# Performance work log

Hardware: AMD Instinct MI355X
Metric: run time of the kernel (lower is better)

The kernel has to match this reference:

```python
import jax, jax.numpy as jnp
import numpy as np

EPS = 1e-6
H = 64
SIGMA = 0.02


def setup_inputs() -> dict:
    key = jax.random.key(0)
    x = jax.random.normal(key, (8, 3, 65536), dtype=jnp.float32)
    return {"x": x}


def reference(x):
    # x: (B, 3, N) in roughly [-1, 1]; map to [0, 1]
    x = jnp.clip(x / 2.0 + 0.5, 0.0, 1.0)
    I = jnp.transpose(x, (0, 2, 1))  # (B, N, 3)
    # intensity scale I_y (intensity_scale=True)
    Iy = jnp.sqrt(jnp.sum(I * I, axis=-1, keepdims=True) + EPS)  # (B, N, 1)
    lin = jnp.linspace(-3.0, 3.0, H, dtype=I.dtype)  # (h,)
    logI = jnp.log(I + EPS)  # (B, N, 3)
    # log-chromaticity coordinates
    Iu = logI - logI[..., jnp.array([1, 0, 0])]  # (B, N, 3)
    Iv = logI - logI[..., jnp.array([2, 2, 1])]  # (B, N, 3)
    # inverse-quadratic kernel over bins: (B, N, 3, h)
    du = jnp.abs(Iu[..., None] - lin)
    dv = jnp.abs(Iv[..., None] - lin)
    ku = 1.0 / (1.0 + jnp.square(du) / (SIGMA ** 2))
    kv = 1.0 / (1.0 + jnp.square(dv) / (SIGMA ** 2))
    wu = Iy[..., None] * ku  # (B, N, 3, h)
    # reduce over pixels via batched outer product -> (B, 3, h, h)
    hists = jnp.einsum('bnch,bncg->bchg', wu, kv)
    return hists / (jnp.sum(hists, axis=(1, 2, 3), keepdims=True) + EPS)
```

## Files before the change

### kernel.cpp

```cpp
#include <hip/hip_runtime.h>
#include <hip/hip_bf16.h>


typedef __bf16 bf16x8 __attribute__((ext_vector_type(8)));
typedef float  f32x4  __attribute__((ext_vector_type(4)));

constexpr int   HBINS = 64;
constexpr float EPSF  = 1e-6f;
constexpr int   BATCH = 8;
constexpr int   NPIX  = 65536;
constexpr int   NBC   = 24;
constexpr int   CHUNKS = 32;
constexpr int   PPC   = NPIX / CHUNKS;
constexpr int   ROUNDS = PPC / 256;
constexpr float BINSTEP  = 300.0f / 63.0f;
constexpr float LOGSCALE = 34.6573590279973f;

__global__ __launch_bounds__(256, 3) void hist_kernel(const float* __restrict__ x,
                                                      float* __restrict__ ws) {
    const int bc   = blockIdx.y;
    const int b    = bc / 3;
    const int c    = bc - b * 3;
    const int t    = threadIdx.x;
    const int lane = t & 63;
    const int w    = t >> 6;
    const int kgrp = lane >> 4;
    const int l16  = lane & 15;

    __shared__ float cu_s[2][256];
    __shared__ float cv_s[2][256];
    __shared__ float iy_s[2][256];
    __shared__ float lhist[HBINS * HBINS];

    for (int i = t; i < HBINS * HBINS; i += 256) lhist[i] = 0.0f;

    f32x4 acc[4][4];
#pragma unroll
    for (int m = 0; m < 4; ++m)
#pragma unroll
        for (int n = 0; n < 4; ++n) acc[m][n] = (f32x4){0.f, 0.f, 0.f, 0.f};

    const float* xr = x + ((size_t)b * 3 + 0) * NPIX;
    const float* xg = x + ((size_t)b * 3 + 1) * NPIX;
    const float* xb = x + ((size_t)b * 3 + 2) * NPIX;
    const int pix0 = blockIdx.x * PPC;

    auto produce = [&](float r, float g, float bl, float& cu, float& cv, float& iy) {
        r  = fminf(fmaxf(fmaf(r,  0.5f, 0.5f), 0.0f), 1.0f);
        g  = fminf(fmaxf(fmaf(g,  0.5f, 0.5f), 0.0f), 1.0f);
        bl = fminf(fmaxf(fmaf(bl, 0.5f, 0.5f), 0.0f), 1.0f);
        const float l2r = __log2f(r  + EPSF);
        const float l2g = __log2f(g  + EPSF);
        const float l2b = __log2f(bl + EPSF);
        float lc, lu, lv;
        if (c == 0)      { lc = l2r; lu = l2g; lv = l2b; }
        else if (c == 1) { lc = l2g; lu = l2r; lv = l2b; }
        else             { lc = l2b; lu = l2r; lv = l2g; }
        cu = (lc - lu) * LOGSCALE;
        cv = (lc - lv) * LOGSCALE;
        iy = __builtin_amdgcn_sqrtf(fmaf(r, r, fmaf(g, g, fmaf(bl, bl, EPSF))));
    };

    {
        float cu, cv, iy;
        produce(xr[pix0 + t], xg[pix0 + t], xb[pix0 + t], cu, cv, iy);
        cu_s[0][t] = cu; cv_s[0][t] = cv; iy_s[0][t] = iy;
    }
    __syncthreads();

    for (int rnd = 0; rnd < ROUNDS; ++rnd) {
        const int cur = rnd & 1;
        const int nxt = cur ^ 1;
        const bool have_next = (rnd + 1 < ROUNDS);

        float rn = 0.f, gn = 0.f, bn = 0.f;
        if (have_next) {
            const int p = pix0 + (rnd + 1) * 256 + t;
            rn = xr[p]; gn = xg[p]; bn = xb[p];
        }

#pragma unroll
        for (int ks = 0; ks < 2; ++ks) {
            const int k0 = w * 64 + ks * 32 + kgrp * 8;
            float cu8[8], cv8[8], iy8[8];
            *(float4*)&cu8[0] = *(const float4*)&cu_s[cur][k0];
            *(float4*)&cu8[4] = *(const float4*)&cu_s[cur][k0 + 4];
            *(float4*)&cv8[0] = *(const float4*)&cv_s[cur][k0];
            *(float4*)&cv8[4] = *(const float4*)&cv_s[cur][k0 + 4];
            *(float4*)&iy8[0] = *(const float4*)&iy_s[cur][k0];
            *(float4*)&iy8[4] = *(const float4*)&iy_s[cur][k0 + 4];

            bf16x8 bfr[4];
#pragma unroll
            for (int n = 0; n < 4; ++n) {
                const float ling = (float)(n * 16 + l16) * BINSTEP - 150.0f;
#pragma unroll
                for (int j = 0; j < 8; ++j) {
                    const float d = cv8[j] - ling;
                    bfr[n][j] = (__bf16)__builtin_amdgcn_rcpf(fmaf(d, d, 1.0f));
                }
            }
#pragma unroll
            for (int m = 0; m < 4; ++m) {
                const float linh = (float)(m * 16 + l16) * BINSTEP - 150.0f;
                bf16x8 af;
#pragma unroll
                for (int j = 0; j < 8; ++j) {
                    const float d = cu8[j] - linh;
                    af[j] = (__bf16)(iy8[j] * __builtin_amdgcn_rcpf(fmaf(d, d, 1.0f)));
                }
#pragma unroll
                for (int n = 0; n < 4; ++n)
                    acc[m][n] = __builtin_amdgcn_mfma_f32_16x16x32_bf16(af, bfr[n], acc[m][n], 0, 0, 0);
            }
        }

        if (have_next) {
            float cu, cv, iy;
            produce(rn, gn, bn, cu, cv, iy);
            cu_s[nxt][t] = cu; cv_s[nxt][t] = cv; iy_s[nxt][t] = iy;
        }
        __syncthreads();
    }

    const int crow = kgrp * 4;
#pragma unroll
    for (int m = 0; m < 4; ++m)
#pragma unroll
        for (int n = 0; n < 4; ++n)
#pragma unroll
            for (int ri = 0; ri < 4; ++ri)
                atomicAdd(&lhist[(m * 16 + crow + ri) * HBINS + n * 16 + l16], acc[m][n][ri]);
    __syncthreads();

    float* gh = ws + (size_t)bc * HBINS * HBINS;
    for (int i = t; i < HBINS * HBINS; i += 256) atomicAdd(&gh[i], lhist[i]);
}

__global__ __launch_bounds__(256) void norm_kernel(const float* __restrict__ ws,
                                                   float* __restrict__ out) {
    const int b = blockIdx.x;
    const float* h = ws  + (size_t)b * 3 * HBINS * HBINS;
    float*       o = out + (size_t)b * 3 * HBINS * HBINS;
    const int t = threadIdx.x;
    const int n = 3 * HBINS * HBINS;

    float s = 0.0f;
    for (int i = t; i < n; i += 256) s += h[i];
#pragma unroll
    for (int off = 32; off > 0; off >>= 1) s += __shfl_down(s, off, 64);

    __shared__ float partial[4];
    if ((t & 63) == 0) partial[t >> 6] = s;
    __syncthreads();
    const float total = partial[0] + partial[1] + partial[2] + partial[3];
    const float inv = 1.0f / (total + EPSF);

    for (int i = t; i < n; i += 256) o[i] = h[i] * inv;
}

extern "C" void kernel_launch(void* const* d_in, const int* in_sizes, int n_in,
                              void* d_out, int out_size, void* d_ws, size_t ws_size,
                              hipStream_t stream) {
    const float* x   = (const float*)d_in[0];
    float*       out = (float*)d_out;
    float*       ws  = (float*)d_ws;

    hipMemsetAsync(ws, 0, (size_t)NBC * HBINS * HBINS * sizeof(float), stream);

    dim3 grid(CHUNKS, NBC);
    hist_kernel<<<grid, 256, 0, stream>>>(x, ws);
    norm_kernel<<<BATCH, 256, 0, stream>>>(ws, out);
}
```

Baseline: 169.7 us.

## Write per-block private histograms instead of global atomics, reduce in norm kernel

Each hist block now stores its 64x64 partial histogram to its own workspace slot with plain vectorized stores, which also removes the memset, when the workspace is large enough. Otherwise atomics are spread over 8 copies per (batch, channel) to cut contention. The norm kernel then sums the copies while normalizing. This removes global atomic contention but makes the norm kernel, which runs only 8 blocks, read 32x more data (about 12.6MB).

```diff
diff --git a/kernel.cpp b/kernel.cpp
--- a/kernel.cpp
+++ b/kernel.cpp
@@ -6,10 +6,12 @@
 typedef float  f32x4  __attribute__((ext_vector_type(4)));
 
 constexpr int   HBINS = 64;
+constexpr int   HB2   = HBINS * HBINS;
 constexpr float EPSF  = 1e-6f;
 constexpr int   BATCH = 8;
 constexpr int   NPIX  = 65536;
 constexpr int   NBC   = 24;
+constexpr int   NCOPY = 8;
 constexpr int   CHUNKS = 32;
 constexpr int   PPC   = NPIX / CHUNKS;
 constexpr int   ROUNDS = PPC / 256;
@@ -17,7 +19,8 @@
 constexpr float LOGSCALE = 34.6573590279973f;
 
 __global__ __launch_bounds__(256, 3) void hist_kernel(const float* __restrict__ x,
-                                                      float* __restrict__ ws) {
+                                                      float* __restrict__ ws,
+                                                      int priv) {
     const int bc   = blockIdx.y;
     const int b    = bc / 3;
     const int c    = bc - b * 3;
@@ -30,9 +33,9 @@
     __shared__ float cu_s[2][256];
     __shared__ float cv_s[2][256];
     __shared__ float iy_s[2][256];
-    __shared__ float lhist[HBINS * HBINS];
+    __shared__ float lhist[HB2];
 
-    for (int i = t; i < HBINS * HBINS; i += 256) lhist[i] = 0.0f;
+    for (int i = t; i < HB2; i += 256) lhist[i] = 0.0f;
 
     f32x4 acc[4][4];
 #pragma unroll
@@ -133,20 +136,27 @@
                 atomicAdd(&lhist[(m * 16 + crow + ri) * HBINS + n * 16 + l16], acc[m][n][ri]);
     __syncthreads();
 
-    float* gh = ws + (size_t)bc * HBINS * HBINS;
-    for (int i = t; i < HBINS * HBINS; i += 256) atomicAdd(&gh[i], lhist[i]);
+    if (priv) {
+        float* gh = ws + ((size_t)bc * CHUNKS + blockIdx.x) * HB2;
+        for (int i = t * 4; i < HB2; i += 1024)
+            *(float4*)&gh[i] = *(const float4*)&lhist[i];
+    } else {
+        float* gh = ws + ((size_t)bc * NCOPY + (blockIdx.x & (NCOPY - 1))) * HB2;
+        for (int i = t; i < HB2; i += 256) atomicAdd(&gh[i], lhist[i]);
+    }
 }
 
 __global__ __launch_bounds__(256) void norm_kernel(const float* __restrict__ ws,
-                                                   float* __restrict__ out) {
+                                                   float* __restrict__ out,
+                                                   int ncopy) {
     const int b = blockIdx.x;
-    const float* h = ws  + (size_t)b * 3 * HBINS * HBINS;
-    float*       o = out + (size_t)b * 3 * HBINS * HBINS;
+    const float* h = ws  + (size_t)b * 3 * ncopy * HB2;
+    float*       o = out + (size_t)b * 3 * HB2;
     const int t = threadIdx.x;
-    const int n = 3 * HBINS * HBINS;
+    const int n = 3 * HB2;
 
     float s = 0.0f;
-    for (int i = t; i < n; i += 256) s += h[i];
+    for (int i = t; i < 3 * ncopy * HB2; i += 256) s += h[i];
 #pragma unroll
     for (int off = 32; off > 0; off >>= 1) s += __shfl_down(s, off, 64);
 
@@ -156,7 +166,14 @@
     const float total = partial[0] + partial[1] + partial[2] + partial[3];
     const float inv = 1.0f / (total + EPSF);
 
-    for (int i = t; i < n; i += 256) o[i] = h[i] * inv;
+    for (int i = t; i < n; i += 256) {
+        const int c  = i >> 12;
+        const int hg = i & 4095;
+        float v = 0.0f;
+        for (int k = 0; k < ncopy; ++k)
+            v += h[((size_t)c * ncopy + k) * HB2 + hg];
+        o[i] = v * inv;
+    }
 }
 
 extern "C" void kernel_launch(void* const* d_in, const int* in_sizes, int n_in,
@@ -166,9 +183,14 @@
     float*       out = (float*)d_out;
     float*       ws  = (float*)d_ws;
 
-    hipMemsetAsync(ws, 0, (size_t)NBC * HBINS * HBINS * sizeof(float), stream);
+    const size_t priv_bytes = (size_t)NBC * CHUNKS * HB2 * sizeof(float);
+    const bool   priv       = ws_size >= priv_bytes;
+
+    if (!priv) {
+        hipMemsetAsync(ws, 0, (size_t)NBC * NCOPY * HB2 * sizeof(float), stream);
+    }
 
     dim3 grid(CHUNKS, NBC);
-    hist_kernel<<<grid, 256, 0, stream>>>(x, ws);
-    norm_kernel<<<BATCH, 256, 0, stream>>>(ws, out);
+    hist_kernel<<<grid, 256, 0, stream>>>(x, ws, priv ? 1 : 0);
+    norm_kernel<<<BATCH, 256, 0, stream>>>(ws, out, priv ? CHUNKS : NCOPY);
 }
```

After: 663.3 us. 3.91x slower.

## Spread global histogram atomics over replicated copies and parallelize normalization

Applied to the files above, without the earlier changes.

The hist kernel now writes its per-block histogram into one of eight replicated copies per (batch, channel), so fewer blocks contend on the same global addresses. A new reduce kernel, spread over 96 blocks, sums the copies, writes the raw histogram to the output and atomically accumulates per-batch totals. A separate scale kernel then normalizes with float4 accesses. This replaces the single 8-block norm kernel, but it adds a launch, a larger memset and extra workspace traffic.

```diff
diff --git a/kernel.cpp b/kernel.cpp
--- a/kernel.cpp
+++ b/kernel.cpp
@@ -6,13 +6,16 @@
 typedef float  f32x4  __attribute__((ext_vector_type(4)));
 
 constexpr int   HBINS = 64;
+constexpr int   HB2   = HBINS * HBINS;
 constexpr float EPSF  = 1e-6f;
 constexpr int   BATCH = 8;
 constexpr int   NPIX  = 65536;
 constexpr int   NBC   = 24;
+constexpr int   NCOPY = 8;
 constexpr int   CHUNKS = 32;
 constexpr int   PPC   = NPIX / CHUNKS;
 constexpr int   ROUNDS = PPC / 256;
+constexpr int   SEGS  = 4;
 constexpr float BINSTEP  = 300.0f / 63.0f;
 constexpr float LOGSCALE = 34.6573590279973f;
 
@@ -30,9 +33,9 @@
     __shared__ float cu_s[2][256];
     __shared__ float cv_s[2][256];
     __shared__ float iy_s[2][256];
-    __shared__ float lhist[HBINS * HBINS];
-
-    for (int i = t; i < HBINS * HBINS; i += 256) lhist[i] = 0.0f;
+    __shared__ float lhist[HB2];
+
+    for (int i = t; i < HB2; i += 256) lhist[i] = 0.0f;
 
     f32x4 acc[4][4];
 #pragma unroll
@@ -133,42 +136,67 @@
                 atomicAdd(&lhist[(m * 16 + crow + ri) * HBINS + n * 16 + l16], acc[m][n][ri]);
     __syncthreads();
 
-    float* gh = ws + (size_t)bc * HBINS * HBINS;
-    for (int i = t; i < HBINS * HBINS; i += 256) atomicAdd(&gh[i], lhist[i]);
-}
-
-__global__ __launch_bounds__(256) void norm_kernel(const float* __restrict__ ws,
-                                                   float* __restrict__ out) {
-    const int b = blockIdx.x;
-    const float* h = ws  + (size_t)b * 3 * HBINS * HBINS;
-    float*       o = out + (size_t)b * 3 * HBINS * HBINS;
+    float* gh = ws + ((size_t)bc * NCOPY + (blockIdx.x & (NCOPY - 1))) * HB2;
+    for (int i = t; i < HB2; i += 256) atomicAdd(&gh[i], lhist[i]);
+}
+
+__global__ __launch_bounds__(256) void reduce_kernel(const float* __restrict__ ws,
+                                                     float* __restrict__ out,
+                                                     float* __restrict__ totals) {
+    const int bc  = blockIdx.x >> 2;
+    const int seg = blockIdx.x & 3;
+    const int b   = bc / 3;
+    const int t   = threadIdx.x;
+    const float* h = ws + (size_t)bc * NCOPY * HB2 + seg * 1024;
+    float*       o = out + (size_t)bc * HB2 + seg * 1024;
+
+    float psum = 0.0f;
+#pragma unroll
+    for (int r = 0; r < 4; ++r) {
+        const int i = r * 256 + t;
+        float v = 0.0f;
+#pragma unroll
+        for (int k = 0; k < NCOPY; ++k) v += h[(size_t)k * HB2 + i];
+        o[i] = v;
+        psum += v;
+    }
+#pragma unroll
+    for (int off = 32; off > 0; off >>= 1) psum += __shfl_down(psum, off, 64);
+    __shared__ float part[4];
+    if ((t & 63) == 0) part[t >> 6] = psum;
+    __syncthreads();
+    if (t == 0)
+        atomicAdd(&totals[b], part[0] + part[1] + part[2] + part[3]);
+}
+
+__global__ __launch_bounds__(256) void scale_kernel(float* __restrict__ out,
+                                                    const float* __restrict__ totals) {
+    const int bc = blockIdx.x;
+    const int b  = bc / 3;
+    const float inv = 1.0f / (totals[b] + EPSF);
+    float* o = out + (size_t)bc * HB2;
     const int t = threadIdx.x;
-    const int n = 3 * HBINS * HBINS;
-
-    float s = 0.0f;
-    for (int i = t; i < n; i += 256) s += h[i];
-#pragma unroll
-    for (int off = 32; off > 0; off >>= 1) s += __shfl_down(s, off, 64);
-
-    __shared__ float partial[4];
-    if ((t & 63) == 0) partial[t >> 6] = s;
-    __syncthreads();
-    const float total = partial[0] + partial[1] + partial[2] + partial[3];
-    const float inv = 1.0f / (total + EPSF);
-
-    for (int i = t; i < n; i += 256) o[i] = h[i] * inv;
+#pragma unroll
+    for (int r = 0; r < 4; ++r) {
+        const int i = (r * 256 + t) * 4;
+        float4 v = *(const float4*)&o[i];
+        v.x *= inv; v.y *= inv; v.z *= inv; v.w *= inv;
+        *(float4*)&o[i] = v;
+    }
 }
 
 extern "C" void kernel_launch(void* const* d_in, const int* in_sizes, int n_in,
                               void* d_out, int out_size, void* d_ws, size_t ws_size,
                               hipStream_t stream) {
-    const float* x   = (const float*)d_in[0];
-    float*       out = (float*)d_out;
-    float*       ws  = (float*)d_ws;
-
-    hipMemsetAsync(ws, 0, (size_t)NBC * HBINS * HBINS * sizeof(float), stream);
+    const float* x      = (const float*)d_in[0];
+    float*       out    = (float*)d_out;
+    float*       ws     = (float*)d_ws;
+    float*       totals = ws + (size_t)NBC * NCOPY * HB2;
+
+    hipMemsetAsync(ws, 0, ((size_t)NBC * NCOPY * HB2 + BATCH) * sizeof(float), stream);
 
     dim3 grid(CHUNKS, NBC);
     hist_kernel<<<grid, 256, 0, stream>>>(x, ws);
-    norm_kernel<<<BATCH, 256, 0, stream>>>(ws, out);
-}
+    reduce_kernel<<<NBC * SEGS, 256, 0, stream>>>(ws, out, totals);
+    scale_kernel<<<NBC, 256, 0, stream>>>(out, totals);
+}
```

Result: faster. 159.4 us (-6.1%).
